# Performance work log

Hardware: AMD Instinct MI355X
Metric: run time of the kernel (lower is better)

The kernel has to match this reference:

```python
import jax, jax.numpy as jnp
import numpy as np

N_EXPERTS = 8
TOP_K = 2
D_MODEL = 1024
D_FF = 4 * D_MODEL

def setup_inputs() -> dict:
    key = jax.random.key(0)
    ks = jax.random.split(key, 5)
    s_in = 1.0 / np.sqrt(D_MODEL)
    s_ff = 1.0 / np.sqrt(D_FF)
    return {
        "x": jax.random.normal(ks[0], (2, 2048, D_MODEL), dtype=jnp.float32),
        "Wr": jax.random.normal(ks[1], (N_EXPERTS, D_MODEL), dtype=jnp.float32) * s_in,
        "W1": jax.random.normal(ks[2], (N_EXPERTS, D_FF, D_MODEL), dtype=jnp.float32) * s_in,
        "W2": jax.random.normal(ks[3], (N_EXPERTS, D_MODEL, D_FF), dtype=jnp.float32) * s_ff,
        "W3": jax.random.normal(ks[4], (N_EXPERTS, D_FF, D_MODEL), dtype=jnp.float32) * s_in,
    }

def reference(x, Wr, W1, W2, W3):
    B, S, D = x.shape
    T = B * S
    xf = x.reshape(T, D)
    logits = xf @ Wr.T                         # [T, E]
    probs = jax.nn.softmax(logits, axis=-1)
    top_p, top_i = jax.lax.top_k(probs, TOP_K)  # [T, K]
    top_p = top_p / jnp.sum(top_p, axis=-1, keepdims=True)
    # per-token combine weight for each expert: [T, E]
    onehot = jax.nn.one_hot(top_i, N_EXPERTS, dtype=x.dtype)  # [T, K, E]
    cw = jnp.einsum('tke,tk->te', onehot, top_p)
    out = jnp.zeros_like(xf)
    for e in range(N_EXPERTS):  # fixed small structural loop over experts
        h = jax.nn.silu(xf @ W1[e].T) * (xf @ W3[e].T)  # [T, F]
        y = h @ W2[e].T                                 # [T, D]
        out = out + cw[:, e:e+1] * y
    importance = jnp.sum(probs, axis=0)                 # [E]
    load = jnp.sum(jnp.sum(onehot, axis=1), axis=0)     # [E]
    aux_loss = jnp.sum(importance * load) * (N_EXPERTS / (T ** 2 + 1e-06))
    return out.reshape(B, S, D), aux_loss
```

## Files before the change

### kernel.cpp

```cpp
#include <hip/hip_runtime.h>

#define T_TOK 4096
#define DM 1024
#define DF 4096
#define NE 8
#define BM 256
#define RCAP 10240
#define MAXT 40
#define MAXT2 80
#define ACH_B 32768
#define CHUNK_B 8192

typedef _Float16 f16x8 __attribute__((ext_vector_type(8)));
typedef float f32x4 __attribute__((ext_vector_type(4)));

#define MFMA16(a, b, c) __builtin_amdgcn_mfma_f32_16x16x32_f16(a, b, c, 0, 0, 0)
#define RAW_BAR() __builtin_amdgcn_s_barrier()
#define VMCNT(n) asm volatile("s_waitcnt vmcnt(" #n ")" ::: "memory")

__device__ __forceinline__ ushort f2h_bits(float f) {
    _Float16 h = (_Float16)f;
    return __builtin_bit_cast(unsigned short, h);
}

__device__ __forceinline__ unsigned int pk2(float a, float b) {
    return __builtin_bit_cast(unsigned int, __builtin_amdgcn_cvt_pkrtz(a, b));
}

__device__ __forceinline__ uint4 pack8(float4 a, float4 b) {
    uint4 r;
    r.x = pk2(a.x, a.y); r.y = pk2(a.z, a.w);
    r.z = pk2(b.x, b.y); r.w = pk2(b.z, b.w);
    return r;
}

__device__ __forceinline__ void gll16(const void* g, void* l) {
    __builtin_amdgcn_global_load_lds(
        (const __attribute__((address_space(1))) unsigned int*)g,
        (__attribute__((address_space(3))) unsigned int*)l, 16, 0, 0);
}

__global__ __launch_bounds__(256) void k_init(float* __restrict__ out,
                                              int* __restrict__ misc,
                                              int* __restrict__ row_tok) {
    int i = blockIdx.x * 256 + threadIdx.x;
    if (i < T_TOK * DM + 1) out[i] = 0.f;
    if (i < RCAP) row_tok[i] = -1;
    if (i < 256) misc[i] = 0;
}

__global__ __launch_bounds__(64) void k_router(const float* __restrict__ x,
                                               const float* __restrict__ Wr,
                                               float* __restrict__ probs,
                                               int* __restrict__ topi,
                                               float* __restrict__ topw,
                                               int* __restrict__ cnt) {
    int t = blockIdx.x;
    int lane = threadIdx.x;
    const float* xr = x + (size_t)t * DM;
    float s[NE];
#pragma unroll
    for (int e = 0; e < NE; e++) s[e] = 0.f;
    for (int j = lane; j < DM; j += 64) {
        float xv = xr[j];
#pragma unroll
        for (int e = 0; e < NE; e++) s[e] += xv * Wr[e * DM + j];
    }
#pragma unroll
    for (int off = 32; off > 0; off >>= 1) {
#pragma unroll
        for (int e = 0; e < NE; e++) s[e] += __shfl_xor(s[e], off, 64);
    }
    if (lane == 0) {
        float mx = s[0];
#pragma unroll
        for (int e = 1; e < NE; e++) mx = fmaxf(mx, s[e]);
        float ex[NE], sum = 0.f;
#pragma unroll
        for (int e = 0; e < NE; e++) { ex[e] = expf(s[e] - mx); sum += ex[e]; }
        float inv = 1.f / sum;
        float p[NE];
#pragma unroll
        for (int e = 0; e < NE; e++) { p[e] = ex[e] * inv; probs[t * NE + e] = p[e]; }
        int i0 = 0;
#pragma unroll
        for (int e = 1; e < NE; e++) if (p[e] > p[i0]) i0 = e;
        int i1 = (i0 == 0) ? 1 : 0;
#pragma unroll
        for (int e = 0; e < NE; e++) if (e != i0 && p[e] > p[i1]) i1 = e;
        float w0 = p[i0], w1 = p[i1], winv = 1.f / (w0 + w1);
        topi[2 * t] = i0;     topw[2 * t] = w0 * winv;
        topi[2 * t + 1] = i1; topw[2 * t + 1] = w1 * winv;
        atomicAdd(&cnt[i0], 1);
        atomicAdd(&cnt[i1], 1);
    }
}

__global__ __launch_bounds__(256) void k_scan(const float* __restrict__ probs,
                                              const int* __restrict__ cnt,
                                              int* __restrict__ poff,
                                              int* __restrict__ texp,
                                              int* __restrict__ texp2,
                                              float* __restrict__ aux_out) {
    __shared__ float red[256 * NE];
    int tid = threadIdx.x;
    float part[NE];
#pragma unroll
    for (int e = 0; e < NE; e++) part[e] = 0.f;
    for (int t = tid; t < T_TOK; t += 256) {
#pragma unroll
        for (int e = 0; e < NE; e++) part[e] += probs[t * NE + e];
    }
#pragma unroll
    for (int e = 0; e < NE; e++) red[tid * NE + e] = part[e];
    __syncthreads();
    for (int s2 = 128; s2 > 0; s2 >>= 1) {
        if (tid < s2) {
#pragma unroll
            for (int e = 0; e < NE; e++) red[tid * NE + e] += red[(tid + s2) * NE + e];
        }
        __syncthreads();
    }
    if (tid == 0) {
        float al = 0.f;
#pragma unroll
        for (int e = 0; e < NE; e++) al += red[e] * (float)cnt[e];
        *aux_out = al * (8.0f / (16777216.0f + 1e-6f));
        int run = 0, tix = 0;
        for (int e = 0; e < NE; e++) {
            poff[e] = run;
            int nt = (cnt[e] + BM - 1) / BM;
            for (int i = 0; i < nt; i++) texp[tix++] = e;
            run += nt * BM;
        }
        for (int j = 0; j < MAXT2; j++) texp2[j] = texp[j >> 1];
    }
}

__global__ __launch_bounds__(256) void k_assign(const int* __restrict__ topi,
                                                const float* __restrict__ topw,
                                                const int* __restrict__ poff,
                                                int* __restrict__ fill,
                                                int* __restrict__ row_tok,
                                                float* __restrict__ row_w) {
    int t = blockIdx.x * 256 + threadIdx.x;
    if (t >= T_TOK) return;
#pragma unroll
    for (int k = 0; k < 2; k++) {
        int e = topi[2 * t + k];
        int pos = atomicAdd(&fill[e], 1);
        int r = poff[e] + pos;
        row_tok[r] = t;
        row_w[r] = topw[2 * t + k];
    }
}

__global__ __launch_bounds__(256) void k_convert(const float* __restrict__ src,
                                                 ushort* __restrict__ dst,
                                                 int row_len) {
    int nk = row_len >> 6;
    int kt = blockIdx.x, rt = blockIdx.y;
    int tid = threadIdx.x;
    int r = tid >> 2, c0 = (tid & 3) * 16;
    const float* s = src + (size_t)(rt * 64 + r) * row_len + kt * 64 + c0;
    float4 v0 = *(const float4*)(s);
    float4 v1 = *(const float4*)(s + 4);
    float4 v2 = *(const float4*)(s + 8);
    float4 v3 = *(const float4*)(s + 12);
    char* chunk = (char*)dst + ((size_t)rt * nk + kt) * CHUNK_B;
    int sw = (r & 7) << 4;
    *(uint4*)(chunk + r * 128 + ((2 * c0) ^ sw)) = pack8(v0, v1);
    *(uint4*)(chunk + r * 128 + ((2 * c0 + 16) ^ sw)) = pack8(v2, v3);
}

__global__ __launch_bounds__(512) void k_gather_t(const float* __restrict__ x,
                                                  const int* __restrict__ row_tok,
                                                  ushort* __restrict__ xg) {
    int kt = blockIdx.x, rt = blockIdx.y;
    int tid = threadIdx.x;
    int r = tid >> 1, c0 = (tid & 1) * 32;
    int tok = row_tok[rt * BM + r];
    char* chunk = (char*)xg + ((size_t)rt * 16 + kt) * ACH_B;
    int sw = (r & 7) << 4;
    if (tok >= 0) {
        const float* s = x + (size_t)tok * DM + kt * 64 + c0;
#pragma unroll
        for (int j = 0; j < 4; j++) {
            float4 va = *(const float4*)(s + j * 8);
            float4 vb = *(const float4*)(s + j * 8 + 4);
            *(uint4*)(chunk + r * 128 + ((c0 * 2 + j * 16) ^ sw)) = pack8(va, vb);
        }
    } else {
        uint4 z = {0, 0, 0, 0};
#pragma unroll
        for (int j = 0; j < 4; j++)
            *(uint4*)(chunk + r * 128 + ((c0 * 2 + j * 16) ^ sw)) = z;
    }
}

__global__ __launch_bounds__(512, 2) void k_g1(const ushort* __restrict__ xg,
                                               const ushort* __restrict__ W1h,
                                               const ushort* __restrict__ W3h,
                                               const int* __restrict__ texp,
                                               ushort* __restrict__ hbuf) {
    __shared__ __align__(16) char lds[131072];
    int b = blockIdx.x;
    int sz = (b & 7) * 160 + (b >> 3);
    int ct = sz / MAXT, rt = sz % MAXT;
    int e = texp[rt];
    int tid = threadIdx.x, lane = tid & 63, wv = tid >> 6;
    int wr = wv >> 1, wc = wv & 1;

    const char* Ac  = (const char*)xg + (size_t)rt * 16 * ACH_B;
    const char* B1c = (const char*)W1h + ((size_t)(e * 64 + ct * 2) * 16) * CHUNK_B;
    const char* B3c = (const char*)W3h + ((size_t)(e * 64 + ct * 2) * 16) * CHUNK_B;

    const f32x4 fz = {0.f, 0.f, 0.f, 0.f};
    f32x4 acc1[4][4], acc3[4][4];
#pragma unroll
    for (int m = 0; m < 4; m++)
#pragma unroll
        for (int n = 0; n < 4; n++) { acc1[m][n] = fz; acc3[m][n] = fz; }

    f16x8 af[4], bf[4];
    int kb_base = (lane >> 4) * 16;

#define ST_A(kt_, b_, h_) {                                                        \
        const char* s_ = Ac + (kt_) * ACH_B + (h_) * 16384 + wv * 2048 + lane * 16; \
        char* d_ = lds + (b_) * 65536 + (h_) * 16384 + wv * 2048;                   \
        gll16(s_, d_); gll16(s_ + 1024, d_ + 1024); }
#define ST_B(Bc_, kt_, b_, off_) {                                                          \
        gll16(Bc_ + (kt_) * 8192 + wv * 1024 + lane * 16,                                    \
              lds + (b_) * 65536 + (off_) + wv * 1024);                                      \
        gll16(Bc_ + 131072 + (kt_) * 8192 + wv * 1024 + lane * 16,                           \
              lds + (b_) * 65536 + (off_) + 8192 + wv * 1024); }
#define DS_A(b_, ks_) _Pragma("unroll") for (int m = 0; m < 4; m++) {              \
        int r_ = wr * 64 + m * 16 + (lane & 15);                                   \
        af[m] = *(const f16x8*)(lds + (b_) * 65536 + r_ * 128 +                    \
                                 (((ks_) * 64 + kb_base) ^ ((r_ & 7) << 4))); }
#define DS_B(b_, off_, ks_) _Pragma("unroll") for (int n = 0; n < 4; n++) {        \
        int c_ = wc * 64 + n * 16 + (lane & 15);                                   \
        bf[n] = *(const f16x8*)(lds + (b_) * 65536 + (off_) + c_ * 128 +           \
                                 (((ks_) * 64 + kb_base) ^ ((c_ & 7) << 4))); }
#define MM(accX) _Pragma("unroll") for (int n = 0; n < 4; n++)                     \
        _Pragma("unroll") for (int m = 0; m < 4; m++)                              \
            accX[m][n] = MFMA16(af[m], bf[n], accX[m][n]);

    ST_A(0, 0, 0); ST_A(0, 0, 1); ST_B(B1c, 0, 0, 32768); ST_B(B3c, 0, 0, 49152);
    VMCNT(2);
    RAW_BAR();

    for (int it = 0; it < 8; ++it) {
        int t1 = 2 * it + 1;
        int t2 = 2 * it + 2;
        DS_A(0, 0); DS_B(0, 32768, 0);
        ST_A(t1, 1, 0);
        RAW_BAR();
        __builtin_amdgcn_s_setprio(1); MM(acc1); __builtin_amdgcn_s_setprio(0);
        VMCNT(2);
        RAW_BAR();
        DS_B(0, 49152, 0);
        ST_A(t1, 1, 1);
        RAW_BAR();
        __builtin_amdgcn_s_setprio(1); MM(acc3); __builtin_amdgcn_s_setprio(0);
        RAW_BAR();
        DS_A(0, 1); DS_B(0, 32768, 1);
        ST_B(B1c, t1, 1, 32768);
        RAW_BAR();
        __builtin_amdgcn_s_setprio(1); MM(acc1); __builtin_amdgcn_s_setprio(0);
        RAW_BAR();
        DS_B(0, 49152, 1);
        ST_B(B3c, t1, 1, 49152);
        RAW_BAR();
        __builtin_amdgcn_s_setprio(1); MM(acc3); __builtin_amdgcn_s_setprio(0);
        VMCNT(2);
        RAW_BAR();
        DS_A(1, 0); DS_B(1, 32768, 0);
        if (it < 7) ST_A(t2, 0, 0);
        RAW_BAR();
        __builtin_amdgcn_s_setprio(1); MM(acc1); __builtin_amdgcn_s_setprio(0);
        if (it < 7) { VMCNT(2); } else { VMCNT(0); }
        RAW_BAR();
        DS_B(1, 49152, 0);
        if (it < 7) ST_A(t2, 0, 1);
        RAW_BAR();
        __builtin_amdgcn_s_setprio(1); MM(acc3); __builtin_amdgcn_s_setprio(0);
        RAW_BAR();
        DS_A(1, 1); DS_B(1, 32768, 1);
        if (it < 7) ST_B(B1c, t2, 0, 32768);
        RAW_BAR();
        __builtin_amdgcn_s_setprio(1); MM(acc1); __builtin_amdgcn_s_setprio(0);
        RAW_BAR();
        DS_B(1, 49152, 1);
        if (it < 7) ST_B(B3c, t2, 0, 49152);
        RAW_BAR();
        __builtin_amdgcn_s_setprio(1); MM(acc3); __builtin_amdgcn_s_setprio(0);
        if (it < 7) { VMCNT(2); }
        RAW_BAR();
    }
#undef ST_A
#undef ST_B
#undef DS_A
#undef DS_B
#undef MM

#pragma unroll
    for (int m = 0; m < 4; m++) {
#pragma unroll
        for (int i = 0; i < 4; i++) {
            int rl = wr * 64 + m * 16 + (lane >> 4) * 4 + i;
            int sw = (rl & 7) << 4;
#pragma unroll
            for (int n = 0; n < 4; n++) {
                int fl = wc * 64 + n * 16 + (lane & 15);
                float a1 = acc1[m][n][i], a3 = acc3[m][n][i];
                float h = (a1 / (1.f + expf(-a1))) * a3;
                char* hc = (char*)hbuf + ((size_t)rt * 64 + ct * 2 + (fl >> 6)) * ACH_B;
                *(ushort*)(hc + rl * 128 + ((2 * (fl & 63)) ^ sw)) = f2h_bits(h);
            }
        }
    }
}

__global__ __launch_bounds__(256, 2) void k_g2(const ushort* __restrict__ hbuf,
                                               const ushort* __restrict__ W2h,
                                               const int* __restrict__ texp2,
                                               const int* __restrict__ row_tok,
                                               const float* __restrict__ row_w,
                                               float* __restrict__ out) {
    __shared__ __align__(16) char lds[65536];
    int b = blockIdx.x;
    int sz = (b & 7) * 80 + (b >> 3);
    int ct = sz / MAXT2, rt2 = sz % MAXT2;
    int e = texp2[rt2];
    int tid = threadIdx.x, lane = tid & 63, wv = tid >> 6;
    int wr = wv >> 1, wc = wv & 1;

    const char* Ac = (const char*)hbuf + ((size_t)(rt2 >> 1) * 64) * ACH_B + (rt2 & 1) * 16384;
    const char* Bc = (const char*)W2h + ((size_t)(e * 16 + ct * 2) * 64) * CHUNK_B;

    const f32x4 fz = {0.f, 0.f, 0.f, 0.f};
    f32x4 acc[4][4];
#pragma unroll
    for (int m = 0; m < 4; m++)
#pragma unroll
        for (int n = 0; n < 4; n++) acc[m][n] = fz;

    f16x8 af[4], bf[4];
    int kb_base = (lane >> 4) * 16;

#define ST2_A(kt_, b_) {                                                            \
        const char* s_ = Ac + (size_t)(kt_) * ACH_B + wv * 4096 + lane * 16;        \
        char* d_ = lds + (b_) * 32768 + wv * 4096;                                  \
        gll16(s_, d_); gll16(s_ + 1024, d_ + 1024);                                 \
        gll16(s_ + 2048, d_ + 2048); gll16(s_ + 3072, d_ + 3072); }
#define ST2_B(kt_, b_) {                                                            \
        gll16(Bc + (kt_) * 8192 + wv * 2048 + lane * 16,                             \
              lds + (b_) * 32768 + 16384 + wv * 2048);                               \
        gll16(Bc + (kt_) * 8192 + wv * 2048 + 1024 + lane * 16,                      \
              lds + (b_) * 32768 + 16384 + wv * 2048 + 1024);                        \
        gll16(Bc + 524288 + (kt_) * 8192 + wv * 2048 + lane * 16,                    \
              lds + (b_) * 32768 + 24576 + wv * 2048);                               \
        gll16(Bc + 524288 + (kt_) * 8192 + wv * 2048 + 1024 + lane * 16,             \
              lds + (b_) * 32768 + 24576 + wv * 2048 + 1024); }
#define DS2_A(b_, ks_) _Pragma("unroll") for (int m = 0; m < 4; m++) {              \
        int r_ = wr * 64 + m * 16 + (lane & 15);                                    \
        af[m] = *(const f16x8*)(lds + (b_) * 32768 + r_ * 128 +                     \
                                 (((ks_) * 64 + kb_base) ^ ((r_ & 7) << 4))); }
#define DS2_B(b_, ks_) _Pragma("unroll") for (int n = 0; n < 4; n++) {              \
        int c_ = wc * 64 + n * 16 + (lane & 15);                                    \
        bf[n] = *(const f16x8*)(lds + (b_) * 32768 + 16384 + c_ * 128 +             \
                                 (((ks_) * 64 + kb_base) ^ ((c_ & 7) << 4))); }
#define MM2() _Pragma("unroll") for (int n = 0; n < 4; n++)                         \
        _Pragma("unroll") for (int m = 0; m < 4; m++)                               \
            acc[m][n] = MFMA16(af[m], bf[n], acc[m][n]);

    ST2_A(0, 0); ST2_B(0, 0);
    VMCNT(0);
    RAW_BAR();

    for (int t = 0; t < 64; ++t) {
        int cb = t & 1;
        DS2_A(cb, 0); DS2_B(cb, 0);
        if (t < 63) ST2_A(t + 1, cb ^ 1);
        RAW_BAR();
        __builtin_amdgcn_s_setprio(1); MM2(); __builtin_amdgcn_s_setprio(0);
        RAW_BAR();
        DS2_A(cb, 1); DS2_B(cb, 1);
        if (t < 63) ST2_B(t + 1, cb ^ 1);
        RAW_BAR();
        __builtin_amdgcn_s_setprio(1); MM2(); __builtin_amdgcn_s_setprio(0);
        if (t < 63) { VMCNT(0); }
        RAW_BAR();
    }
#undef ST2_A
#undef ST2_B
#undef DS2_A
#undef DS2_B
#undef MM2

#pragma unroll
    for (int m = 0; m < 4; m++) {
#pragma unroll
        for (int i = 0; i < 4; i++) {
            int rr = rt2 * 128 + wr * 64 + m * 16 + (lane >> 4) * 4 + i;
            int tok = row_tok[rr];
            if (tok >= 0) {
                float w = row_w[rr];
                float* orow = out + (size_t)tok * DM + ct * 128 + wc * 64 + (lane & 15);
#pragma unroll
                for (int n = 0; n < 4; n++) atomicAdd(&orow[n * 16], w * acc[m][n][i]);
            }
        }
    }
}

extern "C" void kernel_launch(void* const* d_in, const int* in_sizes, int n_in,
                              void* d_out, int out_size, void* d_ws, size_t ws_size,
                              hipStream_t stream) {
    (void)in_sizes; (void)n_in; (void)out_size; (void)ws_size;
    const float* x  = (const float*)d_in[0];
    const float* Wr = (const float*)d_in[1];
    const float* W1 = (const float*)d_in[2];
    const float* W2 = (const float*)d_in[3];
    const float* W3 = (const float*)d_in[4];
    float* out = (float*)d_out;
    char* ws = (char*)d_ws;

    int* misc  = (int*)ws;
    int* cnt   = misc;
    int* fill  = misc + 8;
    int* poff  = misc + 16;
    int* texp  = misc + 24;
    int* texp2 = misc + 64;
    int*    topi    = (int*)(ws + 1024);
    float*  topw    = (float*)(ws + 33792);
    float*  probs   = (float*)(ws + 66560);
    int*    row_tok = (int*)(ws + 197632);
    float*  row_w   = (float*)(ws + 238592);
    ushort* hbuf    = (ushort*)(ws + 279552);
    ushort* W1h     = (ushort*)(ws + 84165632);
    ushort* W3h     = (ushort*)(ws + 151274496);
    ushort* xg      = (ushort*)(ws + 218383360);
    ushort* W2h     = (ushort*)(ws + 218383360);

    k_init<<<(T_TOK * DM + 1 + 255) / 256, 256, 0, stream>>>(out, misc, row_tok);
    k_router<<<T_TOK, 64, 0, stream>>>(x, Wr, probs, topi, topw, cnt);
    k_scan<<<1, 256, 0, stream>>>(probs, cnt, poff, texp, texp2, out + (size_t)T_TOK * DM);
    k_assign<<<(T_TOK + 255) / 256, 256, 0, stream>>>(topi, topw, poff, fill, row_tok, row_w);

    k_convert<<<dim3(16, 512), 256, 0, stream>>>(W1, W1h, DM);
    k_convert<<<dim3(16, 512), 256, 0, stream>>>(W3, W3h, DM);
    k_gather_t<<<dim3(16, MAXT), 512, 0, stream>>>(x, row_tok, xg);
    k_g1<<<32 * MAXT, 512, 0, stream>>>(xg, W1h, W3h, texp, hbuf);
    k_convert<<<dim3(64, 128), 256, 0, stream>>>(W2, W2h, DF);
    k_g2<<<8 * MAXT2, 256, 0, stream>>>(hbuf, W2h, texp2, row_tok, row_w, out);
}
```

Measured before the change: 642.5 us.

## Enlarge second GEMM tile to 256 rows and triple-buffer LDS loads

The down-projection kernel now uses 512-thread blocks covering a full 256-row expert tile instead of two 128-row halves, so each W2 tile loaded into LDS is reused across twice as many rows. The per-stage staging buffer moves from double to triple buffering, with loads issued two iterations ahead and a partial vmcnt wait so global loads overlap more compute. LDS use grows to 144 KB per block and occupancy drops to one block per CU, which may reduce latency hiding. The grid also shrinks by half.

```diff
diff --git a/kernel.cpp b/kernel.cpp
--- a/kernel.cpp
+++ b/kernel.cpp
@@ -7,7 +7,6 @@
 #define BM 256
 #define RCAP 10240
 #define MAXT 40
-#define MAXT2 80
 #define ACH_B 32768
 #define CHUNK_B 8192
 
@@ -100,7 +99,6 @@
                                               const int* __restrict__ cnt,
                                               int* __restrict__ poff,
                                               int* __restrict__ texp,
-                                              int* __restrict__ texp2,
                                               float* __restrict__ aux_out) {
     __shared__ float red[256 * NE];
     int tid = threadIdx.x;
@@ -133,7 +131,6 @@
             for (int i = 0; i < nt; i++) texp[tix++] = e;
             run += nt * BM;
         }
-        for (int j = 0; j < MAXT2; j++) texp2[j] = texp[j >> 1];
     }
 }
 
@@ -322,21 +319,21 @@
     }
 }
 
-__global__ __launch_bounds__(256, 2) void k_g2(const ushort* __restrict__ hbuf,
+__global__ __launch_bounds__(512, 1) void k_g2(const ushort* __restrict__ hbuf,
                                                const ushort* __restrict__ W2h,
-                                               const int* __restrict__ texp2,
+                                               const int* __restrict__ texp,
                                                const int* __restrict__ row_tok,
                                                const float* __restrict__ row_w,
                                                float* __restrict__ out) {
-    __shared__ __align__(16) char lds[65536];
+    __shared__ __align__(16) char lds[147456];
     int b = blockIdx.x;
-    int sz = (b & 7) * 80 + (b >> 3);
-    int ct = sz / MAXT2, rt2 = sz % MAXT2;
-    int e = texp2[rt2];
+    int sz = (b & 7) * MAXT + (b >> 3);
+    int ct = sz / MAXT, rt = sz % MAXT;
+    int e = texp[rt];
     int tid = threadIdx.x, lane = tid & 63, wv = tid >> 6;
     int wr = wv >> 1, wc = wv & 1;
 
-    const char* Ac = (const char*)hbuf + ((size_t)(rt2 >> 1) * 64) * ACH_B + (rt2 & 1) * 16384;
+    const char* Ac = (const char*)hbuf + (size_t)rt * 64 * ACH_B;
     const char* Bc = (const char*)W2h + ((size_t)(e * 16 + ct * 2) * 64) * CHUNK_B;
 
     const f32x4 fz = {0.f, 0.f, 0.f, 0.f};
@@ -349,50 +346,50 @@
     f16x8 af[4], bf[4];
     int kb_base = (lane >> 4) * 16;
 
-#define ST2_A(kt_, b_) {                                                            \
-        const char* s_ = Ac + (size_t)(kt_) * ACH_B + wv * 4096 + lane * 16;        \
-        char* d_ = lds + (b_) * 32768 + wv * 4096;                                  \
-        gll16(s_, d_); gll16(s_ + 1024, d_ + 1024);                                 \
+#define BUF3(t_) (((t_) % 3) * 49152)
+#define ST2_A(kt_) {                                                                 \
+        const char* s_ = Ac + (size_t)(kt_) * ACH_B + wv * 4096 + lane * 16;         \
+        char* d_ = lds + BUF3(kt_) + wv * 4096;                                      \
+        gll16(s_, d_); gll16(s_ + 1024, d_ + 1024);                                  \
         gll16(s_ + 2048, d_ + 2048); gll16(s_ + 3072, d_ + 3072); }
-#define ST2_B(kt_, b_) {                                                            \
-        gll16(Bc + (kt_) * 8192 + wv * 2048 + lane * 16,                             \
-              lds + (b_) * 32768 + 16384 + wv * 2048);                               \
-        gll16(Bc + (kt_) * 8192 + wv * 2048 + 1024 + lane * 16,                      \
-              lds + (b_) * 32768 + 16384 + wv * 2048 + 1024);                        \
-        gll16(Bc + 524288 + (kt_) * 8192 + wv * 2048 + lane * 16,                    \
-              lds + (b_) * 32768 + 24576 + wv * 2048);                               \
-        gll16(Bc + 524288 + (kt_) * 8192 + wv * 2048 + 1024 + lane * 16,             \
-              lds + (b_) * 32768 + 24576 + wv * 2048 + 1024); }
-#define DS2_A(b_, ks_) _Pragma("unroll") for (int m = 0; m < 4; m++) {              \
-        int r_ = wr * 64 + m * 16 + (lane & 15);                                    \
-        af[m] = *(const f16x8*)(lds + (b_) * 32768 + r_ * 128 +                     \
+#define ST2_B(kt_) {                                                                 \
+        gll16(Bc + (size_t)(kt_) * 8192 + wv * 1024 + lane * 16,                     \
+              lds + BUF3(kt_) + 32768 + wv * 1024);                                  \
+        gll16(Bc + 524288 + (size_t)(kt_) * 8192 + wv * 1024 + lane * 16,            \
+              lds + BUF3(kt_) + 40960 + wv * 1024); }
+#define DS2_A(bo_, ks_) _Pragma("unroll") for (int m = 0; m < 4; m++) {              \
+        int r_ = wr * 64 + m * 16 + (lane & 15);                                     \
+        af[m] = *(const f16x8*)(lds + (bo_) + r_ * 128 +                             \
                                  (((ks_) * 64 + kb_base) ^ ((r_ & 7) << 4))); }
-#define DS2_B(b_, ks_) _Pragma("unroll") for (int n = 0; n < 4; n++) {              \
-        int c_ = wc * 64 + n * 16 + (lane & 15);                                    \
-        bf[n] = *(const f16x8*)(lds + (b_) * 32768 + 16384 + c_ * 128 +             \
+#define DS2_B(bo_, ks_) _Pragma("unroll") for (int n = 0; n < 4; n++) {              \
+        int c_ = wc * 64 + n * 16 + (lane & 15);                                     \
+        bf[n] = *(const f16x8*)(lds + (bo_) + 32768 + c_ * 128 +                     \
                                  (((ks_) * 64 + kb_base) ^ ((c_ & 7) << 4))); }
-#define MM2() _Pragma("unroll") for (int n = 0; n < 4; n++)                         \
-        _Pragma("unroll") for (int m = 0; m < 4; m++)                               \
+#define MM2() _Pragma("unroll") for (int n = 0; n < 4; n++)                          \
+        _Pragma("unroll") for (int m = 0; m < 4; m++)                                \
             acc[m][n] = MFMA16(af[m], bf[n], acc[m][n]);
 
-    ST2_A(0, 0); ST2_B(0, 0);
-    VMCNT(0);
+    ST2_A(0); ST2_B(0);
+    ST2_A(1); ST2_B(1);
+    VMCNT(6);
     RAW_BAR();
 
     for (int t = 0; t < 64; ++t) {
-        int cb = t & 1;
-        DS2_A(cb, 0); DS2_B(cb, 0);
-        if (t < 63) ST2_A(t + 1, cb ^ 1);
+        int bo = BUF3(t);
+        DS2_A(bo, 0); DS2_B(bo, 0);
+        if (t < 62) ST2_A(t + 2);
         RAW_BAR();
         __builtin_amdgcn_s_setprio(1); MM2(); __builtin_amdgcn_s_setprio(0);
         RAW_BAR();
-        DS2_A(cb, 1); DS2_B(cb, 1);
-        if (t < 63) ST2_B(t + 1, cb ^ 1);
+        DS2_A(bo, 1); DS2_B(bo, 1);
+        if (t < 62) ST2_B(t + 2);
         RAW_BAR();
         __builtin_amdgcn_s_setprio(1); MM2(); __builtin_amdgcn_s_setprio(0);
-        if (t < 63) { VMCNT(0); }
-        RAW_BAR();
-    }
+        if (t < 62) { VMCNT(6); }
+        else if (t == 62) { VMCNT(0); }
+        RAW_BAR();
+    }
+#undef BUF3
 #undef ST2_A
 #undef ST2_B
 #undef DS2_A
@@ -403,7 +400,7 @@
     for (int m = 0; m < 4; m++) {
 #pragma unroll
         for (int i = 0; i < 4; i++) {
-            int rr = rt2 * 128 + wr * 64 + m * 16 + (lane >> 4) * 4 + i;
+            int rr = rt * BM + wr * 64 + m * 16 + (lane >> 4) * 4 + i;
             int tok = row_tok[rr];
             if (tok >= 0) {
                 float w = row_w[rr];
@@ -432,7 +429,6 @@
     int* fill  = misc + 8;
     int* poff  = misc + 16;
     int* texp  = misc + 24;
-    int* texp2 = misc + 64;
     int*    topi    = (int*)(ws + 1024);
     float*  topw    = (float*)(ws + 33792);
     float*  probs   = (float*)(ws + 66560);
@@ -446,7 +442,7 @@
 
     k_init<<<(T_TOK * DM + 1 + 255) / 256, 256, 0, stream>>>(out, misc, row_tok);
     k_router<<<T_TOK, 64, 0, stream>>>(x, Wr, probs, topi, topw, cnt);
-    k_scan<<<1, 256, 0, stream>>>(probs, cnt, poff, texp, texp2, out + (size_t)T_TOK * DM);
+    k_scan<<<1, 256, 0, stream>>>(probs, cnt, poff, texp, out + (size_t)T_TOK * DM);
     k_assign<<<(T_TOK + 255) / 256, 256, 0, stream>>>(topi, topw, poff, fill, row_tok, row_w);
 
     k_convert<<<dim3(16, 512), 256, 0, stream>>>(W1, W1h, DM);
@@ -454,5 +450,5 @@
     k_gather_t<<<dim3(16, MAXT), 512, 0, stream>>>(x, row_tok, xg);
     k_g1<<<32 * MAXT, 512, 0, stream>>>(xg, W1h, W3h, texp, hbuf);
     k_convert<<<dim3(64, 128), 256, 0, stream>>>(W2, W2h, DF);
-    k_g2<<<8 * MAXT2, 256, 0, stream>>>(hbuf, W2h, texp2, row_tok, row_w, out);
-}
+    k_g2<<<8 * MAXT, 512, 0, stream>>>(hbuf, W2h, texp, row_tok, row_w, out);
+}
```

After: 637.1 us. Within noise of the previous version (-0.8%).
